# Optimization experiments

Hardware: AMD Instinct MI355X
Metric: run time of the kernel (lower is better)

## Reference

```python
import jax, jax.numpy as jnp
import numpy as np

GRID_SIZE = 5
SPLINE_ORDER = 3
IN_FEAT = 320   # 32 * 10
OUT_FEAT = 2048 # 32 * 64
BN_EPS = 1e-3


def make_grid():
    # efficient-kan grid buffer: (in_features, grid_size + 2*spline_order + 1)
    h = 2.0 / GRID_SIZE  # grid_range = [-1, 1]
    g = jnp.arange(-SPLINE_ORDER, GRID_SIZE + SPLINE_ORDER + 1, dtype=jnp.float32) * h - 1.0
    return jnp.broadcast_to(g, (IN_FEAT, g.shape[0]))  # (320, 12)


def b_splines(x, grid):
    # x: (B, In) -> bases: (B, In, grid_size + spline_order)
    x = x[..., None]  # (B, In, 1)
    bases = ((x >= grid[:, :-1]) & (x < grid[:, 1:])).astype(x.dtype)
    for k in range(1, SPLINE_ORDER + 1):
        left = (x - grid[:, : -(k + 1)]) / (grid[:, k:-1] - grid[:, : -(k + 1)])
        right = (grid[:, k + 1:] - x) / (grid[:, k + 1:] - grid[:, 1:-k])
        bases = left * bases[..., :-1] + right * bases[..., 1:]
    return bases


def setup_inputs() -> dict:
    key = jax.random.key(0)
    ks = jax.random.split(key, 8)
    N = 40000
    inputs = jax.random.normal(ks[0], (N, 32, 10), dtype=jnp.float32)
    linear_w = jax.random.normal(ks[1], (64, 10), dtype=jnp.float32) * 0.1
    base_weight = jax.random.normal(ks[2], (OUT_FEAT, IN_FEAT), dtype=jnp.float32) * 0.02
    spline_weight = jax.random.normal(ks[3], (OUT_FEAT, IN_FEAT, GRID_SIZE + SPLINE_ORDER), dtype=jnp.float32) * 0.02
    spline_scaler = jax.random.normal(ks[4], (OUT_FEAT, IN_FEAT), dtype=jnp.float32) * 0.1 + 1.0
    bn_gamma = jax.random.normal(ks[5], (64,), dtype=jnp.float32) * 0.1 + 1.0
    bn_beta = jax.random.normal(ks[6], (64,), dtype=jnp.float32) * 0.1
    bn_mean = jnp.zeros((64,), dtype=jnp.float32)
    bn_var = jax.random.uniform(ks[7], (64,), dtype=jnp.float32, minval=0.5, maxval=1.5)
    return {
        "inputs": inputs,
        "linear_w": linear_w,
        "base_weight": base_weight,
        "spline_weight": spline_weight,
        "spline_scaler": spline_scaler,
        "bn_gamma": bn_gamma,
        "bn_beta": bn_beta,
        "bn_mean": bn_mean,
        "bn_var": bn_var,
    }


def reference(inputs, linear_w, base_weight, spline_weight, spline_scaler,
              bn_gamma, bn_beta, bn_mean, bn_var):
    N = inputs.shape[0]
    # plain linear path: (N, 32, 10) -> (N, 32, 64). (The torch chunking over
    # self.part is mathematically identical to one matmul.)
    x_linear = jnp.einsum('npi,oi->npo', inputs, linear_w)
    # KAN path on flattened pillars: (N, 320)
    xk = inputs.reshape(N, IN_FEAT)
    grid = make_grid()
    base_out = jnp.matmul(jax.nn.silu(xk), base_weight.T)  # (N, 2048)
    bases = b_splines(xk, grid)  # (N, 320, 8)
    scaled_spline_w = (spline_weight * spline_scaler[..., None]).reshape(OUT_FEAT, -1)
    spline_out = jnp.matmul(bases.reshape(N, -1), scaled_spline_w.T)  # (N, 2048)
    x_kan = (base_out + spline_out).reshape(N, 32, 64)
    x = x_linear + x_kan
    # BatchNorm1d over the channel (last) dim, inference mode, eps=1e-3
    inv_std = jax.lax.rsqrt(bn_var + BN_EPS)
    x = (x - bn_mean) * (inv_std * bn_gamma) + bn_beta
    x = jax.nn.relu(x)
    x_max = jnp.max(x, axis=1, keepdims=True)  # (N, 1, 64)
    x_rep = jnp.broadcast_to(x_max, x.shape)   # repeat over 32 points
    return jnp.concatenate([x, x_rep], axis=2)  # (N, 32, 128)
```

## Files before the change

kernel.cpp:

```cpp
#include <hip/hip_runtime.h>
#include <cstdint>
#include <math.h>

#define IN_FEAT 320
#define OUT_FEAT 2048
#define NB 8
#define KSIL 320
#define KTOT 2880
#define BM1 256
#define BN1 128
#define BM 128
#define BN 128
#define BK 32
#define LDA 40
#define BN_EPS 1e-3f
#define A_OFF ((size_t)16 << 20)

typedef __bf16 bf16;
typedef __attribute__((ext_vector_type(8))) __bf16 bf16x8;
typedef __attribute__((ext_vector_type(4))) float f32x4;

__device__ __forceinline__ void bspline8(float xv, float* b) {
    float xc = (xv + 2.2f) * 2.5f;
    float cf = floorf(xc);
    int c = (int)cf;
    float t = xc - cf;
    float omt = 1.0f - t;
    float t2 = t * t, t3 = t2 * t;
    float w0 = omt * omt * omt * (1.0f / 6.0f);
    float w1 = (3.0f * t3 - 6.0f * t2 + 4.0f) * (1.0f / 6.0f);
    float w2 = (-3.0f * t3 + 3.0f * t2 + 3.0f * t + 1.0f) * (1.0f / 6.0f);
    float w3 = t3 * (1.0f / 6.0f);
    if (xc < 0.0f) { w0 = w1 = w2 = w3 = 0.0f; }
#pragma unroll
    for (int j = 0; j < 8; ++j) {
        int d = c - j;
        b[j] = (d == 3) ? w0 : (d == 2) ? w1 : (d == 1) ? w2 : (d == 0) ? w3 : 0.0f;
    }
}

__device__ __forceinline__ bf16x8 pack8(const float* f) {
    bf16x8 v;
#pragma unroll
    for (int j = 0; j < 8; ++j) v[j] = (bf16)f[j];
    return v;
}

__device__ __forceinline__ void gl2lds16(const bf16* g, bf16* l) {
    __builtin_amdgcn_global_load_lds(
        (const __attribute__((address_space(1))) void*)g,
        (__attribute__((address_space(3))) void*)l, 16, 0, 0);
}

__global__ __launch_bounds__(256) void prep_w(const float* __restrict__ bw,
                                              const float* __restrict__ sw,
                                              const float* __restrict__ ss,
                                              bf16* __restrict__ W) {
    const int t = blockIdx.x * 256 + threadIdx.x;
    if (t >= OUT_FEAT * (KTOT / 8)) return;
    const int o = t / (KTOT / 8);
    const int m = t - o * (KTOT / 8);
    const int k0 = m * 8;
    float w[8];
    if (k0 < KSIL) {
        const float* p = &bw[o * IN_FEAT + k0];
#pragma unroll
        for (int u = 0; u < 8; ++u) w[u] = p[u];
    } else {
        const int i = (k0 - KSIL) >> 3;
        const float s = ss[o * IN_FEAT + i];
        const float* p = &sw[(o * IN_FEAT + i) * NB];
#pragma unroll
        for (int u = 0; u < 8; ++u) w[u] = p[u] * s;
    }
    *(bf16x8*)&W[(size_t)o * KTOT + k0] = pack8(w);
}

__global__ __launch_bounds__(256) void prep_a(const float* __restrict__ x,
                                              bf16* __restrict__ A, int total8) {
    const int t = blockIdx.x * 256 + threadIdx.x;
    if (t >= total8) return;
    const int row = t / (IN_FEAT / 8);
    const int f0 = (t - row * (IN_FEAT / 8)) * 8;
    const float4 v0 = *(const float4*)&x[(size_t)row * IN_FEAT + f0];
    const float4 v1 = *(const float4*)&x[(size_t)row * IN_FEAT + f0 + 4];
    float xv[8] = {v0.x, v0.y, v0.z, v0.w, v1.x, v1.y, v1.z, v1.w};
    float sil[8];
#pragma unroll
    for (int u = 0; u < 8; ++u) sil[u] = xv[u] / (1.0f + __expf(-xv[u]));
    bf16* ar = A + (size_t)row * KTOT;
    *(bf16x8*)&ar[f0] = pack8(sil);
#pragma unroll
    for (int u = 0; u < 8; ++u) {
        float b[8];
        bspline8(xv[u], b);
        *(bf16x8*)&ar[KSIL + (f0 + u) * 8] = pack8(b);
    }
}

__global__ __launch_bounds__(512)
void pfn_gemm_ws(const float* __restrict__ x, const bf16* __restrict__ A,
                 const bf16* __restrict__ W, const float* __restrict__ lw,
                 const float* __restrict__ gamma, const float* __restrict__ beta,
                 const float* __restrict__ mean, const float* __restrict__ var,
                 float* __restrict__ out, int N, int nbx) {
    __shared__ bf16 As[BM1 * BK];
    __shared__ bf16 Bs[BN1 * BK];

    const int blk = blockIdx.x;
    const int sid = blk >> 9;
    const int t = blk & 511;
    const int by = t >> 5;
    const int bx = (sid << 5) + (t & 31);
    if (bx >= nbx) return;

    const int row0 = bx * BM1;
    const int col0 = by * BN1;
    const int tid = threadIdx.x;
    const int wave = tid >> 6;
    const int lane = tid & 63;
    const int wr = wave >> 1;
    const int wc = wave & 1;
    const int l15 = lane & 15;
    const int quad = lane >> 4;

    const int r0 = tid >> 2;
    const int s0 = tid & 3;
    const int g0 = s0 ^ ((r0 >> 1) & 3);
    const bf16* a0 = A + (size_t)(row0 + r0) * KTOT + g0 * 8;
    const bf16* a1 = a0 + (size_t)128 * KTOT;
    const bf16* b0 = W + (size_t)(col0 + r0) * KTOT + g0 * 8;
    bf16* lA0 = As + tid * 8;
    bf16* lA1 = As + (tid + 512) * 8;
    bf16* lB0 = Bs + tid * 8;

    const int sfr = quad ^ ((l15 >> 1) & 3);

    f32x4 acc[4][4] = {};

    for (int kc = 0; kc < KTOT; kc += BK) {
        __syncthreads();
        gl2lds16(a0 + kc, lA0);
        gl2lds16(a1 + kc, lA1);
        gl2lds16(b0 + kc, lB0);
        __syncthreads();
        bf16x8 af[4], bv[4];
#pragma unroll
        for (int i = 0; i < 4; ++i)
            af[i] = *(const bf16x8*)&As[(wr * 64 + i * 16 + l15) * BK + sfr * 8];
#pragma unroll
        for (int j = 0; j < 4; ++j)
            bv[j] = *(const bf16x8*)&Bs[(wc * 64 + j * 16 + l15) * BK + sfr * 8];
#pragma unroll
        for (int i = 0; i < 4; ++i)
#pragma unroll
            for (int j = 0; j < 4; ++j)
                acc[i][j] = __builtin_amdgcn_mfma_f32_16x16x32_bf16(af[i], bv[j],
                                                                   acc[i][j], 0, 0, 0);
    }

    const int p = by * 2 + wc;
    float sc[4], sh[4];
#pragma unroll
    for (int j = 0; j < 4; ++j) {
        const int c = j * 16 + l15;
        const float s = rsqrtf(var[c] + BN_EPS) * gamma[c];
        sc[j] = s;
        sh[j] = beta[c] - mean[c] * s;
    }
#pragma unroll
    for (int i = 0; i < 4; ++i) {
#pragma unroll
        for (int reg = 0; reg < 4; ++reg) {
            const int row = row0 + wr * 64 + i * 16 + quad * 4 + reg;
            if (row >= N) continue;
            float xq[10];
            const float* xp = &x[(size_t)row * IN_FEAT + p * 10];
#pragma unroll
            for (int q = 0; q < 10; ++q) xq[q] = xp[q];
#pragma unroll
            for (int j = 0; j < 4; ++j) {
                const int c = j * 16 + l15;
                float v = acc[i][j][reg];
#pragma unroll
                for (int q = 0; q < 10; ++q) v = fmaf(xq[q], lw[c * 10 + q], v);
                v = fmaxf(v * sc[j] + sh[j], 0.0f);
                out[((size_t)row * 32 + p) * 128 + c] = v;
            }
        }
    }
}

template <bool HASW>
__global__ __launch_bounds__(256)
void pfn_gemm(const float* __restrict__ x, const bf16* __restrict__ W,
              const float* __restrict__ bw, const float* __restrict__ sw,
              const float* __restrict__ ss, const float* __restrict__ lw,
              const float* __restrict__ gamma, const float* __restrict__ beta,
              const float* __restrict__ mean, const float* __restrict__ var,
              float* __restrict__ out, int N) {
    __shared__ bf16 As[BM * LDA];
    __shared__ bf16 Bs[BN * LDA];
    const int tid = threadIdx.x;
    const int row0 = blockIdx.x * BM;
    const int col0 = blockIdx.y * BN;
    const int wave = tid >> 6;
    const int lane = tid & 63;
    const int wr = wave >> 1;
    const int wc = wave & 1;
    const int l15 = lane & 15;
    const int quad = lane >> 4;
    f32x4 acc[4][4] = {};
    auto stage_b = [&](int kc) {
        const int ol = tid >> 1;
        const int k0 = (tid & 1) * 16;
        if (HASW) {
            const bf16x8* src = (const bf16x8*)&W[(size_t)(col0 + ol) * KTOT + kc + k0];
            *(bf16x8*)&Bs[ol * LDA + k0] = src[0];
            *(bf16x8*)&Bs[ol * LDA + k0 + 8] = src[1];
        } else {
            const int o = col0 + ol;
#pragma unroll
            for (int u = 0; u < 16; ++u) {
                const int gk = kc + k0 + u;
                float w;
                if (gk < KSIL) {
                    w = bw[o * IN_FEAT + gk];
                } else {
                    const int s = gk - KSIL;
                    const int i = s >> 3, j = s & 7;
                    w = sw[(o * IN_FEAT + i) * NB + j] * ss[o * IN_FEAT + i];
                }
                Bs[ol * LDA + k0 + u] = (bf16)w;
            }
        }
    };
    auto mma_step = [&]() {
        bf16x8 af[4], bv[4];
#pragma unroll
        for (int i = 0; i < 4; ++i)
            af[i] = *(const bf16x8*)&As[(wr * 64 + i * 16 + l15) * LDA + quad * 8];
#pragma unroll
        for (int j = 0; j < 4; ++j)
            bv[j] = *(const bf16x8*)&Bs[(wc * 64 + j * 16 + l15) * LDA + quad * 8];
#pragma unroll
        for (int i = 0; i < 4; ++i)
#pragma unroll
            for (int j = 0; j < 4; ++j)
                acc[i][j] = __builtin_amdgcn_mfma_f32_16x16x32_bf16(af[i], bv[j],
                                                                   acc[i][j], 0, 0, 0);
    };
    for (int kc = 0; kc < KSIL; kc += BK) {
        __syncthreads();
        stage_b(kc);
        {
            const int r = tid >> 1;
            const int k0 = (tid & 1) * 16;
            const int row = row0 + r;
            float v[16];
            if (row < N) {
                const float* xp = &x[(size_t)row * IN_FEAT + kc + k0];
#pragma unroll
                for (int u = 0; u < 16; ++u) {
                    const float xv = xp[u];
                    v[u] = xv / (1.0f + __expf(-xv));
                }
            } else {
#pragma unroll
                for (int u = 0; u < 16; ++u) v[u] = 0.0f;
            }
            *(bf16x8*)&As[r * LDA + k0] = pack8(v);
            *(bf16x8*)&As[r * LDA + k0 + 8] = pack8(v + 8);
        }
        __syncthreads();
        mma_step();
    }
    for (int kc = KSIL; kc < KTOT; kc += BK) {
        __syncthreads();
        stage_b(kc);
        {
            const int i0 = (kc - KSIL) >> 3;
#pragma unroll
            for (int s = 0; s < 2; ++s) {
                const int task = tid + s * 256;
                const int r = task >> 2;
                const int f = task & 3;
                const int row = row0 + r;
                float b[8];
                if (row < N) {
                    bspline8(x[(size_t)row * IN_FEAT + i0 + f], b);
                } else {
#pragma unroll
                    for (int j = 0; j < 8; ++j) b[j] = 0.0f;
                }
                *(bf16x8*)&As[r * LDA + f * 8] = pack8(b);
            }
        }
        __syncthreads();
        mma_step();
    }
    const int p = blockIdx.y * 2 + wc;
    float sc[4], sh[4];
#pragma unroll
    for (int j = 0; j < 4; ++j) {
        const int c = j * 16 + l15;
        const float s = rsqrtf(var[c] + BN_EPS) * gamma[c];
        sc[j] = s;
        sh[j] = beta[c] - mean[c] * s;
    }
#pragma unroll
    for (int i = 0; i < 4; ++i) {
#pragma unroll
        for (int reg = 0; reg < 4; ++reg) {
            const int row = row0 + wr * 64 + i * 16 + quad * 4 + reg;
            if (row >= N) continue;
            float xq[10];
            const float* xp = &x[(size_t)row * IN_FEAT + p * 10];
#pragma unroll
            for (int q = 0; q < 10; ++q) xq[q] = xp[q];
#pragma unroll
            for (int j = 0; j < 4; ++j) {
                const int c = j * 16 + l15;
                float v = acc[i][j][reg];
#pragma unroll
                for (int q = 0; q < 10; ++q) v = fmaf(xq[q], lw[c * 10 + q], v);
                v = fmaxf(v * sc[j] + sh[j], 0.0f);
                out[((size_t)row * 32 + p) * 128 + c] = v;
            }
        }
    }
}

__global__ __launch_bounds__(256) void pfn_maxcat(float* __restrict__ out, int N) {
    const int n = blockIdx.x * 16 + (threadIdx.x >> 4);
    const int q = threadIdx.x & 15;
    if (n >= N) return;
    float* base = out + (size_t)n * 32 * 128 + q * 4;
    f32x4 m = {0.0f, 0.0f, 0.0f, 0.0f};
#pragma unroll
    for (int pp = 0; pp < 32; ++pp) {
        const f32x4 v = *(const f32x4*)&base[pp * 128];
        m[0] = fmaxf(m[0], v[0]);
        m[1] = fmaxf(m[1], v[1]);
        m[2] = fmaxf(m[2], v[2]);
        m[3] = fmaxf(m[3], v[3]);
    }
#pragma unroll
    for (int pp = 0; pp < 32; ++pp)
        *(f32x4*)&base[pp * 128 + 64] = m;
}

extern "C" void kernel_launch(void* const* d_in, const int* in_sizes, int n_in,
                              void* d_out, int out_size, void* d_ws, size_t ws_size,
                              hipStream_t stream) {
    const float* x     = (const float*)d_in[0];
    const float* lw    = (const float*)d_in[1];
    const float* bw    = (const float*)d_in[2];
    const float* sw    = (const float*)d_in[3];
    const float* ss    = (const float*)d_in[4];
    const float* gamma = (const float*)d_in[5];
    const float* beta  = (const float*)d_in[6];
    const float* mean  = (const float*)d_in[7];
    const float* var   = (const float*)d_in[8];
    float* out = (float*)d_out;

    const int N = in_sizes[0] / IN_FEAT;
    const int nbx = (N + BM1 - 1) / BM1;
    const size_t w_bytes = (size_t)OUT_FEAT * KTOT * sizeof(bf16);
    const size_t a_bytes = (size_t)nbx * BM1 * KTOT * sizeof(bf16);

    if (ws_size >= A_OFF + a_bytes) {
        bf16* W = (bf16*)d_ws;
        bf16* A = (bf16*)((char*)d_ws + A_OFF);
        prep_w<<<(OUT_FEAT * (KTOT / 8) + 255) / 256, 256, 0, stream>>>(bw, sw, ss, W);
        const int total8 = N * (IN_FEAT / 8);
        prep_a<<<(total8 + 255) / 256, 256, 0, stream>>>(x, A, total8);
        const int supers = (nbx + 31) / 32;
        pfn_gemm_ws<<<supers * 512, 512, 0, stream>>>(x, A, W, lw, gamma, beta,
                                                      mean, var, out, N, nbx);
    } else if (ws_size >= w_bytes) {
        bf16* W = (bf16*)d_ws;
        prep_w<<<(OUT_FEAT * (KTOT / 8) + 255) / 256, 256, 0, stream>>>(bw, sw, ss, W);
        pfn_gemm<true><<<dim3((N + BM - 1) / BM, OUT_FEAT / BN), 256, 0, stream>>>(
            x, W, bw, sw, ss, lw, gamma, beta, mean, var, out, N);
    } else {
        pfn_gemm<false><<<dim3((N + BM - 1) / BM, OUT_FEAT / BN), 256, 0, stream>>>(
            x, nullptr, bw, sw, ss, lw, gamma, beta, mean, var, out, N);
    }
    pfn_maxcat<<<(N + 15) / 16, 256, 0, stream>>>(out, N);
}
```

Baseline: 1.582 ms.

## Double-buffer LDS and enlarge GEMM tile to 256x256 with BK64

Restructures the workspace GEMM kernel to use a 256x256 output tile with 1024 threads (16 waves), a K-step of 64, and double-buffered LDS. The next K-slice is staged while the current one is computed, which removes one barrier per iteration. The LDS swizzle is widened to 8 groups to match the new layout. The larger tile raises arithmetic intensity per load, at the cost of 128KB of LDS per block, which limits occupancy to one block per CU, and fewer blocks overall.

```diff
diff --git a/kernel.cpp b/kernel.cpp
--- a/kernel.cpp
+++ b/kernel.cpp
@@ -8,7 +8,9 @@
 #define KSIL 320
 #define KTOT 2880
 #define BM1 256
-#define BN1 128
+#define BN1 256
+#define BK1 64
+#define NT1 (KTOT / BK1)
 #define BM 128
 #define BN 128
 #define BK 32
@@ -98,18 +100,18 @@
     }
 }
 
-__global__ __launch_bounds__(512)
+__global__ __launch_bounds__(1024)
 void pfn_gemm_ws(const float* __restrict__ x, const bf16* __restrict__ A,
                  const bf16* __restrict__ W, const float* __restrict__ lw,
                  const float* __restrict__ gamma, const float* __restrict__ beta,
                  const float* __restrict__ mean, const float* __restrict__ var,
                  float* __restrict__ out, int N, int nbx) {
-    __shared__ bf16 As[BM1 * BK];
-    __shared__ bf16 Bs[BN1 * BK];
+    __shared__ bf16 As[2][BM1 * BK1];
+    __shared__ bf16 Bs[2][BN1 * BK1];
 
     const int blk = blockIdx.x;
-    const int sid = blk >> 9;
-    const int t = blk & 511;
+    const int sid = blk >> 8;
+    const int t = blk & 255;
     const int by = t >> 5;
     const int bx = (sid << 5) + (t & 31);
     if (bx >= nbx) return;
@@ -119,47 +121,60 @@
     const int tid = threadIdx.x;
     const int wave = tid >> 6;
     const int lane = tid & 63;
-    const int wr = wave >> 1;
-    const int wc = wave & 1;
+    const int wr = wave >> 2;
+    const int wc = wave & 3;
     const int l15 = lane & 15;
     const int quad = lane >> 4;
 
-    const int r0 = tid >> 2;
-    const int s0 = tid & 3;
-    const int g0 = s0 ^ ((r0 >> 1) & 3);
+    const int r0 = tid >> 3;
+    const int s0 = tid & 7;
+    const int g0 = s0 ^ (r0 & 7);
     const bf16* a0 = A + (size_t)(row0 + r0) * KTOT + g0 * 8;
     const bf16* a1 = a0 + (size_t)128 * KTOT;
     const bf16* b0 = W + (size_t)(col0 + r0) * KTOT + g0 * 8;
-    bf16* lA0 = As + tid * 8;
-    bf16* lA1 = As + (tid + 512) * 8;
-    bf16* lB0 = Bs + tid * 8;
-
-    const int sfr = quad ^ ((l15 >> 1) & 3);
+    const bf16* b1 = b0 + (size_t)128 * KTOT;
+
+    const int h7 = l15 & 7;
 
     f32x4 acc[4][4] = {};
 
-    for (int kc = 0; kc < KTOT; kc += BK) {
+    auto stage = [&](int b, int kc) {
+        gl2lds16(a0 + kc, &As[b][tid * 8]);
+        gl2lds16(a1 + kc, &As[b][(tid + 1024) * 8]);
+        gl2lds16(b0 + kc, &Bs[b][tid * 8]);
+        gl2lds16(b1 + kc, &Bs[b][(tid + 1024) * 8]);
+    };
+    auto compute = [&](int b) {
+#pragma unroll
+        for (int half = 0; half < 2; ++half) {
+            const int sfr = ((half << 2) | quad) ^ h7;
+            bf16x8 af[4], bv[4];
+#pragma unroll
+            for (int i = 0; i < 4; ++i)
+                af[i] = *(const bf16x8*)&As[b][(wr * 64 + i * 16 + l15) * BK1 + sfr * 8];
+#pragma unroll
+            for (int j = 0; j < 4; ++j)
+                bv[j] = *(const bf16x8*)&Bs[b][(wc * 64 + j * 16 + l15) * BK1 + sfr * 8];
+#pragma unroll
+            for (int i = 0; i < 4; ++i)
+#pragma unroll
+                for (int j = 0; j < 4; ++j)
+                    acc[i][j] = __builtin_amdgcn_mfma_f32_16x16x32_bf16(
+                        af[i], bv[j], acc[i][j], 0, 0, 0);
+        }
+    };
+
+    stage(0, 0);
+    __syncthreads();
+    int cur = 0;
+    for (int tt = 0; tt < NT1; ++tt) {
+        if (tt + 1 < NT1) stage(cur ^ 1, (tt + 1) * BK1);
+        compute(cur);
         __syncthreads();
-        gl2lds16(a0 + kc, lA0);
-        gl2lds16(a1 + kc, lA1);
-        gl2lds16(b0 + kc, lB0);
-        __syncthreads();
-        bf16x8 af[4], bv[4];
-#pragma unroll
-        for (int i = 0; i < 4; ++i)
-            af[i] = *(const bf16x8*)&As[(wr * 64 + i * 16 + l15) * BK + sfr * 8];
-#pragma unroll
-        for (int j = 0; j < 4; ++j)
-            bv[j] = *(const bf16x8*)&Bs[(wc * 64 + j * 16 + l15) * BK + sfr * 8];
-#pragma unroll
-        for (int i = 0; i < 4; ++i)
-#pragma unroll
-            for (int j = 0; j < 4; ++j)
-                acc[i][j] = __builtin_amdgcn_mfma_f32_16x16x32_bf16(af[i], bv[j],
-                                                                   acc[i][j], 0, 0, 0);
-    }
-
-    const int p = by * 2 + wc;
+        cur ^= 1;
+    }
+
+    const int p = by * 4 + wc;
     float sc[4], sh[4];
 #pragma unroll
     for (int j = 0; j < 4; ++j) {
@@ -376,8 +391,8 @@
         const int total8 = N * (IN_FEAT / 8);
         prep_a<<<(total8 + 255) / 256, 256, 0, stream>>>(x, A, total8);
         const int supers = (nbx + 31) / 32;
-        pfn_gemm_ws<<<supers * 512, 512, 0, stream>>>(x, A, W, lw, gamma, beta,
-                                                      mean, var, out, N, nbx);
+        pfn_gemm_ws<<<supers * 256, 1024, 0, stream>>>(x, A, W, lw, gamma, beta,
+                                                       mean, var, out, N, nbx);
     } else if (ws_size >= w_bytes) {
         bf16* W = (bf16*)d_ws;
         prep_w<<<(OUT_FEAT * (KTOT / 8) + 255) / 256, 256, 0, stream>>>(bw, sw, ss, W);
```

Result: faster. 1.504 ms (-5.0%).
